# Performance work log

Measured on AMD Instinct MI355X. Metric: run time of the kernel, lower is better.

Reference implementation:

```python
import jax, jax.numpy as jnp
import numpy as np

B = 8192
W = 48            # target-net width
P = 4849          # flat param size of target MLP(1->48->48->48->1)
HW = 96           # hypernet width = 2*W
STEPS = 20
LR = 0.1
B1, B2, EPS = 0.9, 0.999, 1e-8


def setup_inputs() -> dict:
    key = jax.random.key(0)
    ks = jax.random.split(key, 6)
    x = jax.random.normal(ks[0], (B, 1), dtype=jnp.float32)
    c = jax.random.normal(ks[1], (B, 1), dtype=jnp.float32)
    # hypernet params (Linear(2,96) -> relu -> Linear(96,4849)), He-ish scaling
    hw1 = jax.random.normal(ks[2], (HW, 2), dtype=jnp.float32) / jnp.sqrt(2.0)
    hb1 = jax.random.normal(ks[3], (HW,), dtype=jnp.float32) * 0.1
    hw2 = jax.random.normal(ks[4], (P, HW), dtype=jnp.float32) / jnp.sqrt(float(HW))
    hb2 = jax.random.normal(ks[5], (P,), dtype=jnp.float32) * 0.1
    return {"x": x, "c": c, "hw1": hw1, "hb1": hb1, "hw2": hw2, "hb2": hb2}


def _target_apply(p, y):
    # unflatten per tree_flatten order: (w,b) per Linear layer of MLP(1,48,48,48,1)
    w0 = p[0:48].reshape(W, 1);      b0 = p[48:96]
    w1 = p[96:2400].reshape(W, W);   b1 = p[2400:2448]
    w2 = p[2448:4752].reshape(W, W); b2 = p[4752:4800]
    w3 = p[4800:4848].reshape(1, W); b3 = p[4848:4849]
    h = jax.nn.swish(w0 @ y + b0)
    h = jax.nn.swish(w1 @ h + b1)
    h = jax.nn.swish(w2 @ h + b2)
    return jnp.squeeze(w3 @ h + b3)


def _taylor_energy_y(energy_fn, y_target, y_anchor):
    # 2nd-order Taylor expansion via nested JVPs (order_y == 2)
    tangent = y_target - y_anchor

    def grad_energy(y):
        return jax.jvp(energy_fn, (y,), (tangent,))[1]

    e0, term1 = jax.jvp(energy_fn, (y_anchor,), (tangent,))
    _, term2 = jax.jvp(grad_energy, (y_anchor,), (tangent,))
    return e0 + term1 + 0.5 * term2


def _energy(y, p, y_anchor):
    return _taylor_energy_y(lambda yi: _target_apply(p, yi), y, y_anchor)


_grad_fn = jax.vmap(jax.grad(_energy), in_axes=(0, 0, 0))  # grad wrt y only


def reference(x, c, hw1, hb1, hw2, hb2):
    hyper_in = jnp.concatenate([x, c], axis=1)                 # (B, 2)
    h = jax.nn.relu(hyper_in @ hw1.T + hb1)                    # (B, 96)
    flat_params = h @ hw2.T + hb2                              # (B, P)

    y0 = jnp.zeros((x.shape[0], 1), dtype=x.dtype)             # y_mean = 0.0
    m0 = jnp.zeros_like(y0)
    v0 = jnp.zeros_like(y0)

    def step(carry, _):
        y, m, v, t = carry
        g = _grad_fn(y, flat_params, y)  # key=None -> anchor y0 = y_curr
        t = t + 1
        m = B1 * m + (1.0 - B1) * g
        v = B2 * v + (1.0 - B2) * g * g
        mh = m / (1.0 - jnp.power(B1, t))
        vh = v / (1.0 - jnp.power(B2, t))
        y = y - LR * mh / (jnp.sqrt(vh) + EPS)
        return (y, m, v, t), None

    (y_final, _, _, _), _ = jax.lax.scan(
        step, (y0, m0, v0, jnp.asarray(0, jnp.int32)), None, length=STEPS)
    return y_final
```

## Files before the change

kernel.cpp:

```cpp
#include <hip/hip_runtime.h>
#include <cstdint>
#include <cstddef>

#define NB    8192
#define NP    4849
#define NW    48

#define NCH   38

typedef __attribute__((ext_vector_type(8))) _Float16 f16x8;
typedef __attribute__((ext_vector_type(4))) float f32x4;
typedef __attribute__((ext_vector_type(2))) float f32x2;

__device__ __forceinline__ const float* pptr(const float* Pp, int i, int rp) {
  return Pp + ((size_t)(rp >> 7) * NB + i) * 128 + (rp & 127);
}

__device__ __forceinline__ int invperm(int rp) {
  if (rp >= 96 && rp < 2400) {
    int t = rp - 96; int kb = t / 192; int rem = t - kb * 192;
    return 96 + (rem >> 2) * 48 + (kb * 4 + (rem & 3));
  }
  if (rp >= 2448 && rp < 4752) {
    int t = rp - 2448; int kb = t / 192; int rem = t - kb * 192;
    return 2448 + (rem >> 2) * 48 + (kb * 4 + (rem & 3));
  }
  return rp;
}

__global__ __launch_bounds__(256, 2) void hyper_gemm(
    const float* __restrict__ x, const float* __restrict__ c,
    const float* __restrict__ hw1, const float* __restrict__ hb1,
    const float* __restrict__ hw2, const float* __restrict__ hb2,
    float* __restrict__ Pp)
{
  const int t   = threadIdx.x;
  const int i0  = blockIdx.y * 64;
  const int rp0 = blockIdx.x * 128;

  const int lane = t & 63;
  const int wv   = t >> 6;
  const int m16  = lane & 15;
  const int q    = lane >> 4;

  float xv[4], cv[4];
  #pragma unroll
  for (int mt = 0; mt < 4; ++mt) {
    int i = i0 + mt * 16 + m16;
    xv[mt] = x[i]; cv[mt] = c[i];
  }

  const float* wr[2];
  #pragma unroll
  for (int nt = 0; nt < 2; ++nt) {
    int rp = rp0 + wv * 32 + nt * 16 + m16;
    wr[nt] = hw2 + (size_t)(rp < NP ? invperm(rp) : 0) * 96;
  }

  f32x4 acc[4][2];
  #pragma unroll
  for (int mt = 0; mt < 4; ++mt)
    #pragma unroll
    for (int nt = 0; nt < 2; ++nt)
      acc[mt][nt] = (f32x4){0.f, 0.f, 0.f, 0.f};

  #pragma unroll
  for (int ch = 0; ch < 3; ++ch) {
    const int k0 = ch * 32 + q * 8;

    float4 bf0[2], bf1[2];
    #pragma unroll
    for (int nt = 0; nt < 2; ++nt) {
      bf0[nt] = *(const float4*)(wr[nt] + k0);
      bf1[nt] = *(const float4*)(wr[nt] + k0 + 4);
    }

    float4 A0 = *(const float4*)(hw1 + 2 * k0);
    float4 A1 = *(const float4*)(hw1 + 2 * k0 + 4);
    float4 A2 = *(const float4*)(hw1 + 2 * k0 + 8);
    float4 A3 = *(const float4*)(hw1 + 2 * k0 + 12);
    float4 B0 = *(const float4*)(hb1 + k0);
    float4 B1 = *(const float4*)(hb1 + k0 + 4);
    float w0k[8] = {A0.x,A0.z,A1.x,A1.z,A2.x,A2.z,A3.x,A3.z};
    float w1k[8] = {A0.y,A0.w,A1.y,A1.w,A2.y,A2.w,A3.y,A3.w};
    float bk[8]  = {B0.x,B0.y,B0.z,B0.w,B1.x,B1.y,B1.z,B1.w};

    f16x8 ah[4], al[4];
    #pragma unroll
    for (int mt = 0; mt < 4; ++mt) {
      #pragma unroll
      for (int j = 0; j < 8; ++j) {
        float h = fmaf(xv[mt], w0k[j], fmaf(cv[mt], w1k[j], bk[j]));
        h = h > 0.f ? h : 0.f;
        _Float16 hi = (_Float16)h;
        float r = h - (float)hi;
        ah[mt][j] = hi;
        al[mt][j] = (_Float16)r;
      }
    }

    f16x8 bh[2], bl[2];
    #pragma unroll
    for (int nt = 0; nt < 2; ++nt) {
      float fv[8] = {bf0[nt].x,bf0[nt].y,bf0[nt].z,bf0[nt].w,
                     bf1[nt].x,bf1[nt].y,bf1[nt].z,bf1[nt].w};
      #pragma unroll
      for (int e = 0; e < 8; ++e) {
        _Float16 hi = (_Float16)fv[e];
        float r = fv[e] - (float)hi;
        bh[nt][e] = hi;
        bl[nt][e] = (_Float16)r;
      }
    }

    #pragma unroll
    for (int mt = 0; mt < 4; ++mt)
      #pragma unroll
      for (int nt = 0; nt < 2; ++nt) {
        acc[mt][nt] = __builtin_amdgcn_mfma_f32_16x16x32_f16(al[mt], bl[nt], acc[mt][nt], 0, 0, 0);
        acc[mt][nt] = __builtin_amdgcn_mfma_f32_16x16x32_f16(ah[mt], bl[nt], acc[mt][nt], 0, 0, 0);
        acc[mt][nt] = __builtin_amdgcn_mfma_f32_16x16x32_f16(al[mt], bh[nt], acc[mt][nt], 0, 0, 0);
        acc[mt][nt] = __builtin_amdgcn_mfma_f32_16x16x32_f16(ah[mt], bh[nt], acc[mt][nt], 0, 0, 0);
      }
  }

  float* cbase = Pp + (size_t)blockIdx.x * NB * 128;
  #pragma unroll
  for (int nt = 0; nt < 2; ++nt) {
    int off = wv * 32 + nt * 16 + m16;
    int rp  = rp0 + off;
    if (rp < NP) {
      float bias = hb2[invperm(rp)];
      #pragma unroll
      for (int mt = 0; mt < 4; ++mt)
        #pragma unroll
        for (int r = 0; r < 4; ++r) {
          int i = i0 + mt * 16 + q * 4 + r;
          cbase[(size_t)i * 128 + off] = acc[mt][nt][r] + bias;
        }
    }
  }
}

__device__ __forceinline__ float rcp_nr(float d) {
  float r = __builtin_amdgcn_rcpf(d);
  return fmaf(-d, r, 2.f) * r;
}

__global__ __launch_bounds__(256, 3) void adam_inner(
    const float* __restrict__ Pp, float* __restrict__ out)
{
  __shared__ __align__(16) float hd[4][2][96];

  const int lane = threadIdx.x & 63;
  const int wv   = threadIdx.x >> 6;
  const int i    = blockIdx.x * 4 + wv;
  const bool act = lane < NW;

  float* buf0 = &hd[wv][0][0];
  float* buf1 = &hd[wv][1][0];

  float w0  = act ? *pptr(Pp, i, lane)        : 0.f;
  float b0  = act ? *pptr(Pp, i, 48 + lane)   : 0.f;
  float b1v = act ? *pptr(Pp, i, 2400 + lane) : 0.f;
  float b2v = act ? *pptr(Pp, i, 4752 + lane) : 0.f;
  float w3  = act ? *pptr(Pp, i, 4800 + lane) : 0.f;

  f32x2 w1p[24], w2p[24];
  #pragma unroll
  for (int kb = 0; kb < 12; ++kb) {
    float4 q1 = *(const float4*)pptr(Pp, i, 96 + kb * 192 + lane * 4);
    w1p[2 * kb]     = (f32x2){q1.x, q1.y};
    w1p[2 * kb + 1] = (f32x2){q1.z, q1.w};
    float4 q2 = *(const float4*)pptr(Pp, i, 2448 + kb * 192 + lane * 4);
    w2p[2 * kb]     = (f32x2){q2.x, q2.y};
    w2p[2 * kb + 1] = (f32x2){q2.z, q2.w};
  }

  float y = 0.f, m = 0.f, v = 0.f;
  float b1t = 1.f, b2t = 1.f;

  #pragma unroll 1
  for (int t = 0; t < 20; ++t) {
    float z  = fmaf(w0, y, b0);
    float e  = fminf(__expf(-z), 8.0e37f);
    float s  = rcp_nr(1.f + e);
    float h  = z * s;
    float dh = fmaf(z * s, 1.f - s, s) * w0;
    if (act) { buf0[lane] = h; buf0[48 + lane] = dh; }

    f32x2 zz1a = (f32x2){b1v, 0.f}, zz1b = (f32x2){0.f, 0.f};
    f32x2 dd1a = (f32x2){0.f, 0.f}, dd1b = (f32x2){0.f, 0.f};
    #pragma unroll
    for (int kk = 0; kk < 12; ++kk) {
      float4 ph = *(const float4*)(buf0 + 4 * kk);
      float4 pd = *(const float4*)(buf0 + 48 + 4 * kk);
      zz1a = __builtin_elementwise_fma(w1p[2 * kk],     (f32x2){ph.x, ph.y}, zz1a);
      zz1b = __builtin_elementwise_fma(w1p[2 * kk + 1], (f32x2){ph.z, ph.w}, zz1b);
      dd1a = __builtin_elementwise_fma(w1p[2 * kk],     (f32x2){pd.x, pd.y}, dd1a);
      dd1b = __builtin_elementwise_fma(w1p[2 * kk + 1], (f32x2){pd.z, pd.w}, dd1b);
    }
    float z1  = (zz1a.x + zz1a.y) + (zz1b.x + zz1b.y);
    float dz1 = (dd1a.x + dd1a.y) + (dd1b.x + dd1b.y);

    e  = fminf(__expf(-z1), 8.0e37f);
    s  = rcp_nr(1.f + e);
    h  = z1 * s;
    dh = fmaf(z1 * s, 1.f - s, s) * dz1;
    if (act) { buf1[lane] = h; buf1[48 + lane] = dh; }

    f32x2 zz2a = (f32x2){b2v, 0.f}, zz2b = (f32x2){0.f, 0.f};
    f32x2 dd2a = (f32x2){0.f, 0.f}, dd2b = (f32x2){0.f, 0.f};
    #pragma unroll
    for (int kk = 0; kk < 12; ++kk) {
      float4 ph = *(const float4*)(buf1 + 4 * kk);
      float4 pd = *(const float4*)(buf1 + 48 + 4 * kk);
      zz2a = __builtin_elementwise_fma(w2p[2 * kk],     (f32x2){ph.x, ph.y}, zz2a);
      zz2b = __builtin_elementwise_fma(w2p[2 * kk + 1], (f32x2){ph.z, ph.w}, zz2b);
      dd2a = __builtin_elementwise_fma(w2p[2 * kk],     (f32x2){pd.x, pd.y}, dd2a);
      dd2b = __builtin_elementwise_fma(w2p[2 * kk + 1], (f32x2){pd.z, pd.w}, dd2b);
    }
    float z2  = (zz2a.x + zz2a.y) + (zz2b.x + zz2b.y);
    float dz2 = (dd2a.x + dd2a.y) + (dd2b.x + dd2b.y);

    e  = fminf(__expf(-z2), 8.0e37f);
    s  = rcp_nr(1.f + e);
    dh = fmaf(z2 * s, 1.f - s, s) * dz2;

    float tg = act ? w3 * dh : 0.f;
    #pragma unroll
    for (int off = 1; off < 64; off <<= 1) tg += __shfl_xor(tg, off, 64);
    float g = tg;

    m = fmaf(0.9f,   m, 0.1f   * g);
    v = fmaf(0.999f, v, 0.001f * g * g);
    b1t *= 0.9f; b2t *= 0.999f;
    float mh  = m * rcp_nr(1.f - b1t);
    float vh  = v * rcp_nr(1.f - b2t);
    float den = __builtin_amdgcn_sqrtf(vh) + 1e-8f;
    y -= 0.1f * mh * rcp_nr(den);
  }

  if (lane == 0) out[i] = y;
}

extern "C" void kernel_launch(void* const* d_in, const int* in_sizes, int n_in,
                              void* d_out, int out_size, void* d_ws, size_t ws_size,
                              hipStream_t stream) {
  const float* x   = (const float*)d_in[0];
  const float* c   = (const float*)d_in[1];
  const float* hw1 = (const float*)d_in[2];
  const float* hb1 = (const float*)d_in[3];
  const float* hw2 = (const float*)d_in[4];
  const float* hb2 = (const float*)d_in[5];
  float* Pp  = (float*)d_ws;
  float* out = (float*)d_out;

  dim3 gridB(38, 128);
  hyper_gemm<<<gridB, dim3(256), 0, stream>>>(x, c, hw1, hb1, hw2, hb2, Pp);
  adam_inner<<<dim3(2048), dim3(256), 0, stream>>>(Pp, out);
}
```

Baseline: 233.6 us.

## Make hyper GEMM persistent over M tiles, reusing split-fp16 weight fragments

The hyper_gemm grid drops from 128 to 16 blocks along the batch dimension. Each block now loops over several 64-row batch tiles, and the hw2 weight fragments plus their fp16 hi/lo split and bias are loaded and converted once, then kept in registers. This removes repeated global loads and conversions of the weights but raises register pressure and cuts the number of blocks. Separately, the adam_inner launch bound drops from 3 to 2 blocks per CU, which lets the compiler use more registers per thread.

```diff
diff --git a/kernel.cpp b/kernel.cpp
--- a/kernel.cpp
+++ b/kernel.cpp
@@ -5,8 +5,8 @@
 #define NB    8192
 #define NP    4849
 #define NW    48
-
 #define NCH   38
+#define GY    16
 
 typedef __attribute__((ext_vector_type(8))) _Float16 f16x8;
 typedef __attribute__((ext_vector_type(4))) float f32x4;
@@ -34,110 +34,112 @@
     const float* __restrict__ hw2, const float* __restrict__ hb2,
     float* __restrict__ Pp)
 {
-  const int t   = threadIdx.x;
-  const int i0  = blockIdx.y * 64;
-  const int rp0 = blockIdx.x * 128;
-
+  const int t    = threadIdx.x;
   const int lane = t & 63;
   const int wv   = t >> 6;
   const int m16  = lane & 15;
   const int q    = lane >> 4;
-
-  float xv[4], cv[4];
-  #pragma unroll
-  for (int mt = 0; mt < 4; ++mt) {
-    int i = i0 + mt * 16 + m16;
-    xv[mt] = x[i]; cv[mt] = c[i];
-  }
+  const int rp0  = blockIdx.x * 128;
 
   const float* wr[2];
+  float bias[2];
   #pragma unroll
   for (int nt = 0; nt < 2; ++nt) {
     int rp = rp0 + wv * 32 + nt * 16 + m16;
-    wr[nt] = hw2 + (size_t)(rp < NP ? invperm(rp) : 0) * 96;
-  }
-
-  f32x4 acc[4][2];
-  #pragma unroll
-  for (int mt = 0; mt < 4; ++mt)
-    #pragma unroll
-    for (int nt = 0; nt < 2; ++nt)
-      acc[mt][nt] = (f32x4){0.f, 0.f, 0.f, 0.f};
-
+    int r  = (rp < NP) ? invperm(rp) : 0;
+    wr[nt]   = hw2 + (size_t)r * 96;
+    bias[nt] = (rp < NP) ? hb2[r] : 0.f;
+  }
+
+  f16x8 bh[3][2], bl[3][2];
   #pragma unroll
   for (int ch = 0; ch < 3; ++ch) {
     const int k0 = ch * 32 + q * 8;
-
-    float4 bf0[2], bf1[2];
     #pragma unroll
     for (int nt = 0; nt < 2; ++nt) {
-      bf0[nt] = *(const float4*)(wr[nt] + k0);
-      bf1[nt] = *(const float4*)(wr[nt] + k0 + 4);
-    }
-
-    float4 A0 = *(const float4*)(hw1 + 2 * k0);
-    float4 A1 = *(const float4*)(hw1 + 2 * k0 + 4);
-    float4 A2 = *(const float4*)(hw1 + 2 * k0 + 8);
-    float4 A3 = *(const float4*)(hw1 + 2 * k0 + 12);
-    float4 B0 = *(const float4*)(hb1 + k0);
-    float4 B1 = *(const float4*)(hb1 + k0 + 4);
-    float w0k[8] = {A0.x,A0.z,A1.x,A1.z,A2.x,A2.z,A3.x,A3.z};
-    float w1k[8] = {A0.y,A0.w,A1.y,A1.w,A2.y,A2.w,A3.y,A3.w};
-    float bk[8]  = {B0.x,B0.y,B0.z,B0.w,B1.x,B1.y,B1.z,B1.w};
-
-    f16x8 ah[4], al[4];
-    #pragma unroll
-    for (int mt = 0; mt < 4; ++mt) {
-      #pragma unroll
-      for (int j = 0; j < 8; ++j) {
-        float h = fmaf(xv[mt], w0k[j], fmaf(cv[mt], w1k[j], bk[j]));
-        h = h > 0.f ? h : 0.f;
-        _Float16 hi = (_Float16)h;
-        float r = h - (float)hi;
-        ah[mt][j] = hi;
-        al[mt][j] = (_Float16)r;
-      }
-    }
-
-    f16x8 bh[2], bl[2];
-    #pragma unroll
-    for (int nt = 0; nt < 2; ++nt) {
-      float fv[8] = {bf0[nt].x,bf0[nt].y,bf0[nt].z,bf0[nt].w,
-                     bf1[nt].x,bf1[nt].y,bf1[nt].z,bf1[nt].w};
+      float4 f0 = *(const float4*)(wr[nt] + k0);
+      float4 f1 = *(const float4*)(wr[nt] + k0 + 4);
+      float fv[8] = {f0.x,f0.y,f0.z,f0.w,f1.x,f1.y,f1.z,f1.w};
       #pragma unroll
       for (int e = 0; e < 8; ++e) {
         _Float16 hi = (_Float16)fv[e];
         float r = fv[e] - (float)hi;
-        bh[nt][e] = hi;
-        bl[nt][e] = (_Float16)r;
+        bh[ch][nt][e] = hi;
+        bl[ch][nt][e] = (_Float16)r;
       }
     }
-
+  }
+
+  float* cbase = Pp + (size_t)blockIdx.x * NB * 128;
+
+  for (int mtile = blockIdx.y; mtile < 128; mtile += GY) {
+    const int i0 = mtile * 64;
+
+    float xv[4], cv[4];
+    #pragma unroll
+    for (int mt = 0; mt < 4; ++mt) {
+      int i = i0 + mt * 16 + m16;
+      xv[mt] = x[i]; cv[mt] = c[i];
+    }
+
+    f32x4 acc[4][2];
     #pragma unroll
     for (int mt = 0; mt < 4; ++mt)
       #pragma unroll
-      for (int nt = 0; nt < 2; ++nt) {
-        acc[mt][nt] = __builtin_amdgcn_mfma_f32_16x16x32_f16(al[mt], bl[nt], acc[mt][nt], 0, 0, 0);
-        acc[mt][nt] = __builtin_amdgcn_mfma_f32_16x16x32_f16(ah[mt], bl[nt], acc[mt][nt], 0, 0, 0);
-        acc[mt][nt] = __builtin_amdgcn_mfma_f32_16x16x32_f16(al[mt], bh[nt], acc[mt][nt], 0, 0, 0);
-        acc[mt][nt] = __builtin_amdgcn_mfma_f32_16x16x32_f16(ah[mt], bh[nt], acc[mt][nt], 0, 0, 0);
+      for (int nt = 0; nt < 2; ++nt)
+        acc[mt][nt] = (f32x4){0.f, 0.f, 0.f, 0.f};
+
+    #pragma unroll
+    for (int ch = 0; ch < 3; ++ch) {
+      const int k0 = ch * 32 + q * 8;
+
+      float4 A0 = *(const float4*)(hw1 + 2 * k0);
+      float4 A1 = *(const float4*)(hw1 + 2 * k0 + 4);
+      float4 A2 = *(const float4*)(hw1 + 2 * k0 + 8);
+      float4 A3 = *(const float4*)(hw1 + 2 * k0 + 12);
+      float4 B0 = *(const float4*)(hb1 + k0);
+      float4 B1 = *(const float4*)(hb1 + k0 + 4);
+      float w0k[8] = {A0.x,A0.z,A1.x,A1.z,A2.x,A2.z,A3.x,A3.z};
+      float w1k[8] = {A0.y,A0.w,A1.y,A1.w,A2.y,A2.w,A3.y,A3.w};
+      float bk[8]  = {B0.x,B0.y,B0.z,B0.w,B1.x,B1.y,B1.z,B1.w};
+
+      f16x8 ah[4], al[4];
+      #pragma unroll
+      for (int mt = 0; mt < 4; ++mt) {
+        #pragma unroll
+        for (int j = 0; j < 8; ++j) {
+          float h = fmaf(xv[mt], w0k[j], fmaf(cv[mt], w1k[j], bk[j]));
+          h = h > 0.f ? h : 0.f;
+          _Float16 hi = (_Float16)h;
+          float r = h - (float)hi;
+          ah[mt][j] = hi;
+          al[mt][j] = (_Float16)r;
+        }
       }
-  }
-
-  float* cbase = Pp + (size_t)blockIdx.x * NB * 128;
-  #pragma unroll
-  for (int nt = 0; nt < 2; ++nt) {
-    int off = wv * 32 + nt * 16 + m16;
-    int rp  = rp0 + off;
-    if (rp < NP) {
-      float bias = hb2[invperm(rp)];
+
       #pragma unroll
       for (int mt = 0; mt < 4; ++mt)
         #pragma unroll
-        for (int r = 0; r < 4; ++r) {
-          int i = i0 + mt * 16 + q * 4 + r;
-          cbase[(size_t)i * 128 + off] = acc[mt][nt][r] + bias;
+        for (int nt = 0; nt < 2; ++nt) {
+          acc[mt][nt] = __builtin_amdgcn_mfma_f32_16x16x32_f16(al[mt], bl[ch][nt], acc[mt][nt], 0, 0, 0);
+          acc[mt][nt] = __builtin_amdgcn_mfma_f32_16x16x32_f16(ah[mt], bl[ch][nt], acc[mt][nt], 0, 0, 0);
+          acc[mt][nt] = __builtin_amdgcn_mfma_f32_16x16x32_f16(al[mt], bh[ch][nt], acc[mt][nt], 0, 0, 0);
+          acc[mt][nt] = __builtin_amdgcn_mfma_f32_16x16x32_f16(ah[mt], bh[ch][nt], acc[mt][nt], 0, 0, 0);
         }
+    }
+
+    #pragma unroll
+    for (int nt = 0; nt < 2; ++nt) {
+      int off = wv * 32 + nt * 16 + m16;
+      if (rp0 + off < NP) {
+        #pragma unroll
+        for (int mt = 0; mt < 4; ++mt)
+          #pragma unroll
+          for (int r = 0; r < 4; ++r) {
+            int i = i0 + mt * 16 + q * 4 + r;
+            cbase[(size_t)i * 128 + off] = acc[mt][nt][r] + bias[nt];
+          }
+      }
     }
   }
 }
@@ -147,7 +149,7 @@
   return fmaf(-d, r, 2.f) * r;
 }
 
-__global__ __launch_bounds__(256, 3) void adam_inner(
+__global__ __launch_bounds__(256, 2) void adam_inner(
     const float* __restrict__ Pp, float* __restrict__ out)
 {
   __shared__ __align__(16) float hd[4][2][96];
@@ -256,7 +258,7 @@
   float* Pp  = (float*)d_ws;
   float* out = (float*)d_out;
 
-  dim3 gridB(38, 128);
+  dim3 gridB(NCH, GY);
   hyper_gemm<<<gridB, dim3(256), 0, stream>>>(x, c, hw1, hb1, hw2, hb2, Pp);
   adam_inner<<<dim3(2048), dim3(256), 0, stream>>>(Pp, out);
 }
```

Result: faster. 228.4 us (-2.2%).
